# Performance work log

Hardware: AMD Instinct MI355X
Metric: run time of the kernel (lower is better)

## Reference

```python
import jax, jax.numpy as jnp
import numpy as np

N = 100000   # nodes
E = 1600000  # edges (avg degree 16)
D = 128      # feature dim (layer_sizes = [128, 128, 128])


def setup_inputs() -> dict:
    key = jax.random.key(0)
    ks = jax.random.split(key, 8)
    s = 1.0 / np.sqrt(D)  # glorot-ish scale for linear weights
    return {
        "x": jax.random.normal(ks[0], (N, D), jnp.float32),
        "edge_index": jax.random.randint(ks[1], (2, E), 0, N, dtype=jnp.int32),
        "perturb_first": jax.random.normal(ks[2], (N, D), jnp.float32) * 0.01,
        "perturb_last": jax.random.normal(ks[3], (N, D), jnp.float32) * 0.01,
        "W1": jax.random.normal(ks[4], (D, D), jnp.float32) * s,
        "b1": jnp.zeros((D,), jnp.float32),
        "W2": jax.random.normal(ks[5], (D, D), jnp.float32) * s,
        "b2": jnp.zeros((D,), jnp.float32),
    }


def reference(x, edge_index, perturb_first, perturb_last, W1, b1, W2, b2):
    n = x.shape[0]
    # PyG GCNConv: add self-loops, symmetric deg^{-1/2} normalization.
    loop = jnp.arange(n, dtype=edge_index.dtype)
    src = jnp.concatenate([edge_index[0], loop])  # [E+N]
    dst = jnp.concatenate([edge_index[1], loop])  # [E+N]
    deg = jax.ops.segment_sum(jnp.ones(dst.shape[0], x.dtype), dst, num_segments=n)
    dinv = jnp.where(deg > 0, 1.0 / jnp.sqrt(deg), 0.0)
    norm = (dinv[src] * dinv[dst])[:, None]  # [E+N, 1]

    def gcn_conv(h, W, b):
        h = h @ W.T                                   # linear (bias-free), [N, D]
        msg = h[src] * norm                           # gather + scale, [E+N, D]
        out = jax.ops.segment_sum(msg, dst, num_segments=n)  # scatter-add
        return out + b

    # forward only runs model[0] and model[3] (the two GCNConv layers);
    # norms and PReLU are skipped by the original forward.
    h = gcn_conv(x, W1, b1) + perturb_first
    out = gcn_conv(h, W2, b2) + perturb_last
    return out
```

## Files before the change

### kernel.cpp

```cpp
#include <hip/hip_runtime.h>
#include <math.h>

#define D 128
#define WS_PAD 132

typedef short bf16x8 __attribute__((ext_vector_type(8)));
typedef float f32x4 __attribute__((ext_vector_type(4)));

__device__ __forceinline__ unsigned short f2bf(float f) {
  unsigned u = __float_as_uint(f);
  u += 0x7FFFu + ((u >> 16) & 1u);
  return (unsigned short)(u >> 16);
}

__device__ __forceinline__ float bf2f(unsigned short h) {
  return __uint_as_float(((unsigned)h) << 16);
}

__device__ __forceinline__ float bflo(unsigned u) { return __uint_as_float(u << 16); }
__device__ __forceinline__ float bfhi(unsigned u) { return __uint_as_float(u & 0xFFFF0000u); }


__global__ __launch_bounds__(256) void wprep_kernel(const float* __restrict__ W2,
                                                    unsigned short* __restrict__ W2bf,
                                                    const float* __restrict__ W1,
                                                    unsigned short* __restrict__ W1h,
                                                    unsigned short* __restrict__ W1l) {
  int which = blockIdx.x;
  if (which < 8) {
    int t = which * 256 + threadIdx.x;
    #pragma unroll
    for (int q = 0; q < 2; ++q) {
      int idx = t + q * 2048;
      float4 w = ((const float4*)W2)[idx];
      ushort4 o;
      o.x = f2bf(w.x); o.y = f2bf(w.y); o.z = f2bf(w.z); o.w = f2bf(w.w);
      ((ushort4*)W2bf)[idx] = o;
    }
  } else {
    int t = (which - 8) * 256 + threadIdx.x;
    #pragma unroll
    for (int q = 0; q < 2; ++q) {
      int idx = t + q * 2048;
      float4 w = ((const float4*)W1)[idx];
      ushort4 hi, lo;
      hi.x = f2bf(w.x); lo.x = f2bf(w.x - bf2f(hi.x));
      hi.y = f2bf(w.y); lo.y = f2bf(w.y - bf2f(hi.y));
      hi.z = f2bf(w.z); lo.z = f2bf(w.z - bf2f(hi.z));
      hi.w = f2bf(w.w); lo.w = f2bf(w.w - bf2f(hi.w));
      ((ushort4*)W1h)[idx] = hi;
      ((ushort4*)W1l)[idx] = lo;
    }
  }
}


#define FUSED_GRID 2048
#define G1_PITCH 136

__global__ __launch_bounds__(256) void count_gemm1_kernel(
    const int* __restrict__ dst, int E, int* __restrict__ deg, int* __restrict__ rank,
    const float* __restrict__ X,
    const unsigned short* __restrict__ W1h, const unsigned short* __restrict__ W1l,
    unsigned short* __restrict__ H, int n) {
  __shared__ unsigned short Ths[32 * G1_PITCH];
  __shared__ unsigned short Tls[32 * G1_PITCH];
  int sub = blockIdx.x & 7;
  if (sub < 4) {
    int cb = (blockIdx.x >> 3) * 4 + sub;
    const int T4 = 1024 * 256 * 4;
    int t = cb * 256 + threadIdx.x;
    const bool al16 = ((E & 3) == 0);
    for (int e0 = t * 4; e0 < E; e0 += T4) {
      if (e0 + 4 <= E && al16) {
        int4 d = *(const int4*)(dst + e0);
        int r0 = atomicAdd(&deg[d.x], 1);
        int r1 = atomicAdd(&deg[d.y], 1);
        int r2 = atomicAdd(&deg[d.z], 1);
        int r3 = atomicAdd(&deg[d.w], 1);
        *(int4*)(rank + e0) = make_int4(r0, r1, r2, r3);
      } else {
        for (int e = e0; e < E && e < e0 + 4; ++e) rank[e] = atomicAdd(&deg[dst[e]], 1);
      }
    }
  } else {
    int gb = (blockIdx.x >> 3) * 4 + (sub - 4);
    const int tid = threadIdx.x;
    const int wv = tid >> 6;
    const int lane = tid & 63;
    const int m = lane & 15;
    const int quad = lane >> 4;
    const int mt = wv >> 1;
    const int ntb = (wv & 1) * 4;
    const int ntiles = (n + 31) >> 5;

    for (int tile = gb; tile < ntiles; tile += 1024) {
      const int row0 = tile << 5;
      const int rows_here = min(32, n - row0);
      __syncthreads();
      {
        const float4* Xg = (const float4*)(X + (size_t)row0 * D);
        int tmax = rows_here * 32;
        for (int t = tid; t < tmax; t += 256) {
          float4 xv = Xg[t];
          int r = t >> 5, c4 = (t & 31) << 2;
          ushort4 hi, lo;
          hi.x = f2bf(xv.x); lo.x = f2bf(xv.x - bf2f(hi.x));
          hi.y = f2bf(xv.y); lo.y = f2bf(xv.y - bf2f(hi.y));
          hi.z = f2bf(xv.z); lo.z = f2bf(xv.z - bf2f(hi.z));
          hi.w = f2bf(xv.w); lo.w = f2bf(xv.w - bf2f(hi.w));
          *(ushort4*)&Ths[r * G1_PITCH + c4] = hi;
          *(ushort4*)&Tls[r * G1_PITCH + c4] = lo;
        }
      }
      __syncthreads();

      f32x4 acc0 = {0.f, 0.f, 0.f, 0.f};
      f32x4 acc1 = {0.f, 0.f, 0.f, 0.f};
      f32x4 acc2 = {0.f, 0.f, 0.f, 0.f};
      f32x4 acc3 = {0.f, 0.f, 0.f, 0.f};
      #pragma unroll
      for (int s = 0; s < 4; ++s) {
        int k = (s << 5) + (quad << 3);
        bf16x8 ah = *(const bf16x8*)&Ths[(mt * 16 + m) * G1_PITCH + k];
        bf16x8 al = *(const bf16x8*)&Tls[(mt * 16 + m) * G1_PITCH + k];
        bf16x8 bh0 = *(const bf16x8*)&W1h[(size_t)((ntb + 0) * 16 + m) * 128 + k];
        bf16x8 bl0 = *(const bf16x8*)&W1l[(size_t)((ntb + 0) * 16 + m) * 128 + k];
        acc0 = __builtin_amdgcn_mfma_f32_16x16x32_bf16(ah, bh0, acc0, 0, 0, 0);
        acc0 = __builtin_amdgcn_mfma_f32_16x16x32_bf16(al, bh0, acc0, 0, 0, 0);
        acc0 = __builtin_amdgcn_mfma_f32_16x16x32_bf16(ah, bl0, acc0, 0, 0, 0);
        bf16x8 bh1 = *(const bf16x8*)&W1h[(size_t)((ntb + 1) * 16 + m) * 128 + k];
        bf16x8 bl1 = *(const bf16x8*)&W1l[(size_t)((ntb + 1) * 16 + m) * 128 + k];
        acc1 = __builtin_amdgcn_mfma_f32_16x16x32_bf16(ah, bh1, acc1, 0, 0, 0);
        acc1 = __builtin_amdgcn_mfma_f32_16x16x32_bf16(al, bh1, acc1, 0, 0, 0);
        acc1 = __builtin_amdgcn_mfma_f32_16x16x32_bf16(ah, bl1, acc1, 0, 0, 0);
        bf16x8 bh2 = *(const bf16x8*)&W1h[(size_t)((ntb + 2) * 16 + m) * 128 + k];
        bf16x8 bl2 = *(const bf16x8*)&W1l[(size_t)((ntb + 2) * 16 + m) * 128 + k];
        acc2 = __builtin_amdgcn_mfma_f32_16x16x32_bf16(ah, bh2, acc2, 0, 0, 0);
        acc2 = __builtin_amdgcn_mfma_f32_16x16x32_bf16(al, bh2, acc2, 0, 0, 0);
        acc2 = __builtin_amdgcn_mfma_f32_16x16x32_bf16(ah, bl2, acc2, 0, 0, 0);
        bf16x8 bh3 = *(const bf16x8*)&W1h[(size_t)((ntb + 3) * 16 + m) * 128 + k];
        bf16x8 bl3 = *(const bf16x8*)&W1l[(size_t)((ntb + 3) * 16 + m) * 128 + k];
        acc3 = __builtin_amdgcn_mfma_f32_16x16x32_bf16(ah, bh3, acc3, 0, 0, 0);
        acc3 = __builtin_amdgcn_mfma_f32_16x16x32_bf16(al, bh3, acc3, 0, 0, 0);
        acc3 = __builtin_amdgcn_mfma_f32_16x16x32_bf16(ah, bl3, acc3, 0, 0, 0);
      }
      #pragma unroll
      for (int r = 0; r < 4; ++r) {
        int row = mt * 16 + (quad << 2) + r;
        int g = row0 + row;
        if (g < n) {
          H[(size_t)g * D + (ntb + 0) * 16 + m] = f2bf(acc0[r]);
          H[(size_t)g * D + (ntb + 1) * 16 + m] = f2bf(acc1[r]);
          H[(size_t)g * D + (ntb + 2) * 16 + m] = f2bf(acc2[r]);
          H[(size_t)g * D + (ntb + 3) * 16 + m] = f2bf(acc3[r]);
        }
      }
    }
  }
}


__global__ __launch_bounds__(256) void fill_kernel(const int* __restrict__ src,
                                                   const int* __restrict__ dst,
                                                   const int* __restrict__ ptr,
                                                   const int* __restrict__ rank,
                                                   int* __restrict__ csr, int E) {
  const int T8 = FUSED_GRID * 256 * 8;
  int t = blockIdx.x * 256 + threadIdx.x;
  const bool al16 = ((E & 3) == 0);
  for (int e0 = t * 8; e0 < E; e0 += T8) {
    if (e0 + 8 <= E && al16) {
      int4 d0 = ((const int4*)(dst + e0))[0];
      int4 d1 = ((const int4*)(dst + e0))[1];
      int4 s0 = ((const int4*)(src + e0))[0];
      int4 s1 = ((const int4*)(src + e0))[1];
      int4 r0 = ((const int4*)(rank + e0))[0];
      int4 r1 = ((const int4*)(rank + e0))[1];
      csr[ptr[d0.x] + r0.x] = s0.x;
      csr[ptr[d0.y] + r0.y] = s0.y;
      csr[ptr[d0.z] + r0.z] = s0.z;
      csr[ptr[d0.w] + r0.w] = s0.w;
      csr[ptr[d1.x] + r1.x] = s1.x;
      csr[ptr[d1.y] + r1.y] = s1.y;
      csr[ptr[d1.z] + r1.z] = s1.z;
      csr[ptr[d1.w] + r1.w] = s1.w;
    } else {
      for (int e = e0; e < E && e < e0 + 8; ++e)
        csr[ptr[dst[e]] + rank[e]] = src[e];
    }
  }
}


__global__ __launch_bounds__(256) void scan_blocksum_kernel(const int* __restrict__ deg, int n,
                                                            int* __restrict__ blockSums) {
  __shared__ int sm[256];
  int t = threadIdx.x;
  int i = blockIdx.x * 256 + t;
  sm[t] = (i < n) ? deg[i] : 0;
  __syncthreads();
  for (int off = 128; off > 0; off >>= 1) {
    if (t < off) sm[t] += sm[t + off];
    __syncthreads();
  }
  if (t == 0) blockSums[blockIdx.x] = sm[0];
}

__global__ __launch_bounds__(512) void scan_top_kernel(int* __restrict__ blockSums, int nb) {
  __shared__ int sm[512];
  int t = threadIdx.x;
  int v = (t < nb) ? blockSums[t] : 0;
  sm[t] = v;
  __syncthreads();
  for (int off = 1; off < 512; off <<= 1) {
    int x = (t >= off) ? sm[t - off] : 0;
    __syncthreads();
    sm[t] += x;
    __syncthreads();
  }
  if (t < nb) blockSums[t] = sm[t] - v;
}

__global__ __launch_bounds__(256) void scan_write_kernel(const int* __restrict__ deg, int n,
                                                         const int* __restrict__ blockSums,
                                                         int* __restrict__ ptr,
                                                         float* __restrict__ dinv) {
  __shared__ int sm[256];
  int t = threadIdx.x;
  int i = blockIdx.x * 256 + t;
  int v = (i < n) ? deg[i] : 0;
  sm[t] = v;
  __syncthreads();
  for (int off = 1; off < 256; off <<= 1) {
    int x = (t >= off) ? sm[t - off] : 0;
    __syncthreads();
    sm[t] += x;
    __syncthreads();
  }
  if (i < n) {
    int ex = blockSums[blockIdx.x] + sm[t] - v;
    ptr[i] = ex;
    dinv[i] = 1.0f / sqrtf((float)(v + 1));
    if (i == n - 1) ptr[n] = ex + v;
  }
}


__device__ __forceinline__ void gemm_body(const float* __restrict__ X,
                                          const float* __restrict__ W,
                                          const float* __restrict__ dinv,
                                          unsigned short* __restrict__ H, int n,
                                          int bid, int nblocks,
                                          float* __restrict__ Ws, float* __restrict__ Xs) {
  const int tid = threadIdx.x;
  const int tx = tid & 31;
  const int ty = tid >> 5;
  const int ntiles = (n + 31) >> 5;

  for (int tile = bid; tile < ntiles; tile += nblocks) {
    const int row0 = tile << 5;
    const int rows_here = min(32, n - row0);
    __syncthreads();
    {
      const float4* Xg = (const float4*)(X + (size_t)row0 * D);
      int tmax = rows_here * 32;
      for (int t = tid; t < tmax; t += 256) ((float4*)Xs)[t] = Xg[t];
    }
    float acc[4][4] = {{0.f}};
    #pragma unroll
    for (int kt = 0; kt < 128; kt += 64) {
      __syncthreads();
      for (int t = tid; t < 2048; t += 256) {
        int j  = t >> 4;
        int k4 = (t & 15) << 2;
        float4 w = ((const float4*)W)[j * 32 + (kt >> 2) + (t & 15)];
        Ws[(k4 + 0) * WS_PAD + j] = w.x;
        Ws[(k4 + 1) * WS_PAD + j] = w.y;
        Ws[(k4 + 2) * WS_PAD + j] = w.z;
        Ws[(k4 + 3) * WS_PAD + j] = w.w;
      }
      __syncthreads();
      #pragma unroll 4
      for (int k = 0; k < 64; ++k) {
        float4 w = *(const float4*)&Ws[k * WS_PAD + (tx << 2)];
        #pragma unroll
        for (int r = 0; r < 4; ++r) {
          float xv = Xs[(ty + 8 * r) * 128 + (kt + k)];
          acc[r][0] += xv * w.x;
          acc[r][1] += xv * w.y;
          acc[r][2] += xv * w.z;
          acc[r][3] += xv * w.w;
        }
      }
    }
    #pragma unroll
    for (int r = 0; r < 4; ++r) {
      int row = row0 + ty + 8 * r;
      if (row < n) {
        float s = dinv[row];
        unsigned h0 = f2bf(s * acc[r][0]);
        unsigned h1 = f2bf(s * acc[r][1]);
        unsigned h2 = f2bf(s * acc[r][2]);
        unsigned h3 = f2bf(s * acc[r][3]);
        ((uint2*)(H + (size_t)row * D))[tx] = make_uint2(h0 | (h1 << 16), h2 | (h3 << 16));
      }
    }
  }
}


__global__ __launch_bounds__(256) void count_legacy_kernel(const int* __restrict__ dst, int E,
                                                           int* __restrict__ deg) {
  int e = blockIdx.x * 256 + threadIdx.x;
  if (e < E) atomicAdd(&deg[dst[e]], 1);
}

__global__ __launch_bounds__(256) void fused_fill_gemm_kernel(
    const int* __restrict__ src, const int* __restrict__ dst,
    int* __restrict__ ptr, int* __restrict__ csr, int E,
    const float* __restrict__ X, const float* __restrict__ W,
    const float* __restrict__ dinv, unsigned short* __restrict__ H, int n) {
  __shared__ float Ws[64 * WS_PAD];
  __shared__ float Xs[32 * 128];
  int sub = blockIdx.x & 7;
  if (sub < 2) {
    int fb = (blockIdx.x >> 3) * 2 + sub;
    int stride = 512 * 256;
    for (int e = fb * 256 + threadIdx.x; e < E; e += stride) {
      int d = dst[e];
      int pos = atomicAdd(&ptr[d], 1);
      csr[pos] = src[e];
    }
  } else {
    int gb = (blockIdx.x >> 3) * 6 + (sub - 2);
    gemm_body(X, W, dinv, H, n, gb, 1536, Ws, Xs);
  }
}

__global__ __launch_bounds__(256) void gemm128_kernel(const float* __restrict__ X,
                                                      const float* __restrict__ W,
                                                      const float* __restrict__ dinv,
                                                      unsigned short* __restrict__ H, int n) {
  __shared__ float Ws[64 * WS_PAD];
  __shared__ float Xs[32 * 128];
  gemm_body(X, W, dinv, H, n, blockIdx.x, gridDim.x, Ws, Xs);
}

__device__ __forceinline__ void gather_row_legacy(const int* __restrict__ csr, int start, int end,
                                                  const unsigned* __restrict__ Hu,
                                                  int i, int lane, float& ax, float& ay) {
  unsigned v = Hu[(size_t)i * 64 + lane];
  ax = __uint_as_float(v << 16);
  ay = __uint_as_float(v & 0xFFFF0000u);
  for (int e = start; e < end; ++e) {
    unsigned w = Hu[(size_t)csr[e] * 64 + lane];
    ax += __uint_as_float(w << 16);
    ay += __uint_as_float(w & 0xFFFF0000u);
  }
}

__global__ __launch_bounds__(256, 8) void gather_kernel_old(const int* __restrict__ csr,
                                                            const int* __restrict__ rend,
                                                            const float* __restrict__ dinv,
                                                            const unsigned* __restrict__ Hu,
                                                            const float* __restrict__ bias,
                                                            const float* __restrict__ perturb,
                                                            float* __restrict__ out, int n) {
  int i = (blockIdx.x << 2) + (threadIdx.x >> 6);
  if (i >= n) return;
  int lane = threadIdx.x & 63;
  int start = (i == 0) ? 0 : rend[i - 1];
  float ax, ay;
  gather_row_legacy(csr, start, rend[i], Hu, i, lane, ax, ay);
  float di = dinv[i];
  float2 p = ((const float2*)(perturb + (size_t)i * D))[lane];
  float2 o;
  o.x = bias[2 * lane + 0] + p.x + di * ax;
  o.y = bias[2 * lane + 1] + p.y + di * ay;
  ((float2*)(out + (size_t)i * D))[lane] = o;
}


__device__ __forceinline__ void gather_quad(const int* __restrict__ csr, int start, int end,
                                            const uint4* __restrict__ Hu4, int i, int sub,
                                            float acc[8]) {
  uint4 v = Hu4[(size_t)i * 16 + sub];
  acc[0] = bflo(v.x); acc[1] = bfhi(v.x);
  acc[2] = bflo(v.y); acc[3] = bfhi(v.y);
  acc[4] = bflo(v.z); acc[5] = bfhi(v.z);
  acc[6] = bflo(v.w); acc[7] = bfhi(v.w);
  int e = start;
  while (__ballot(e < end)) {
    uint4 w0 = {0u, 0u, 0u, 0u}, w1 = {0u, 0u, 0u, 0u};
    if (e < end)     w0 = Hu4[(size_t)csr[e] * 16 + sub];
    if (e + 1 < end) w1 = Hu4[(size_t)csr[e + 1] * 16 + sub];
    acc[0] += bflo(w0.x); acc[1] += bfhi(w0.x);
    acc[2] += bflo(w0.y); acc[3] += bfhi(w0.y);
    acc[4] += bflo(w0.z); acc[5] += bfhi(w0.z);
    acc[6] += bflo(w0.w); acc[7] += bfhi(w0.w);
    acc[0] += bflo(w1.x); acc[1] += bfhi(w1.x);
    acc[2] += bflo(w1.y); acc[3] += bfhi(w1.y);
    acc[4] += bflo(w1.z); acc[5] += bfhi(w1.z);
    acc[6] += bflo(w1.w); acc[7] += bfhi(w1.w);
    e += 2;
  }
}

__device__ __forceinline__ void gather_quad_w(const int* __restrict__ csr, int start, int end,
                                              const uint4* __restrict__ Hu4,
                                              const float* __restrict__ dinv,
                                              int i, int sub, float acc[8]) {
  float ds = dinv[i];
  uint4 v = Hu4[(size_t)i * 16 + sub];
  acc[0] = ds * bflo(v.x); acc[1] = ds * bfhi(v.x);
  acc[2] = ds * bflo(v.y); acc[3] = ds * bfhi(v.y);
  acc[4] = ds * bflo(v.z); acc[5] = ds * bfhi(v.z);
  acc[6] = ds * bflo(v.w); acc[7] = ds * bfhi(v.w);
  int e = start;
  while (__ballot(e < end)) {
    uint4 w0 = {0u, 0u, 0u, 0u}, w1 = {0u, 0u, 0u, 0u};
    float d0 = 0.f, d1 = 0.f;
    if (e < end)     { int j = csr[e];     w0 = Hu4[(size_t)j * 16 + sub]; d0 = dinv[j]; }
    if (e + 1 < end) { int j = csr[e + 1]; w1 = Hu4[(size_t)j * 16 + sub]; d1 = dinv[j]; }
    acc[0] += d0 * bflo(w0.x); acc[1] += d0 * bfhi(w0.x);
    acc[2] += d0 * bflo(w0.y); acc[3] += d0 * bfhi(w0.y);
    acc[4] += d0 * bflo(w0.z); acc[5] += d0 * bfhi(w0.z);
    acc[6] += d0 * bflo(w0.w); acc[7] += d0 * bfhi(w0.w);
    acc[0] += d1 * bflo(w1.x); acc[1] += d1 * bfhi(w1.x);
    acc[2] += d1 * bflo(w1.y); acc[3] += d1 * bfhi(w1.y);
    acc[4] += d1 * bflo(w1.z); acc[5] += d1 * bfhi(w1.z);
    acc[6] += d1 * bflo(w1.w); acc[7] += d1 * bfhi(w1.w);
    e += 2;
  }
}


__global__ __launch_bounds__(256, 8) void gather_kernel(const int* __restrict__ csr,
                                                        const int* __restrict__ rptr,
                                                        const float* __restrict__ dinv,
                                                        const unsigned* __restrict__ Hu,
                                                        const float* __restrict__ bias,
                                                        const float* __restrict__ perturb,
                                                        float* __restrict__ out, int n) {
  const int lane = threadIdx.x & 63;
  const int g = lane >> 4;
  const int sub = lane & 15;
  int i = (blockIdx.x << 4) + ((threadIdx.x >> 6) << 2) + g;
  bool valid = i < n;
  int ic = valid ? i : (n - 1);
  int start = rptr[ic];
  int end = valid ? rptr[ic + 1] : start;
  float acc[8];
  gather_quad(csr, start, end, (const uint4*)Hu, ic, sub, acc);
  if (valid) {
    float di = dinv[i];
    float4 b0 = *(const float4*)&bias[sub * 8];
    float4 b1 = *(const float4*)&bias[sub * 8 + 4];
    float4 p0 = *(const float4*)&perturb[(size_t)i * D + sub * 8];
    float4 p1 = *(const float4*)&perturb[(size_t)i * D + sub * 8 + 4];
    float4 o0, o1;
    o0.x = b0.x + p0.x + di * acc[0];
    o0.y = b0.y + p0.y + di * acc[1];
    o0.z = b0.z + p0.z + di * acc[2];
    o0.w = b0.w + p0.w + di * acc[3];
    o1.x = b1.x + p1.x + di * acc[4];
    o1.y = b1.y + p1.y + di * acc[5];
    o1.z = b1.z + p1.z + di * acc[6];
    o1.w = b1.w + p1.w + di * acc[7];
    *(float4*)&out[(size_t)i * D + sub * 8] = o0;
    *(float4*)&out[(size_t)i * D + sub * 8 + 4] = o1;
  }
}


#define GG_PITCH 136

__global__ __launch_bounds__(512, 8) void gather_gemm_kernel(
    const int* __restrict__ csr, const int* __restrict__ rptr,
    const float* __restrict__ dinv, const unsigned* __restrict__ Hu,
    const float* __restrict__ bias, const float* __restrict__ perturb,
    const unsigned short* __restrict__ W2bf, unsigned short* __restrict__ H2, int n) {
  __shared__ unsigned short Ts[32 * GG_PITCH];
  const int tid = threadIdx.x;
  const int wv = tid >> 6;
  const int lane = tid & 63;
  const int base = blockIdx.x << 5;

  {
    const int g = lane >> 4;
    const int sub = lane & 15;
    int row_in_block = (wv << 2) + g;
    int i = base + row_in_block;
    bool valid = i < n;
    int ic = valid ? i : (n - 1);
    int start = rptr[ic];
    int end = valid ? rptr[ic + 1] : start;
    float acc[8];
    gather_quad_w(csr, start, end, (const uint4*)Hu, dinv, ic, sub, acc);
    if (valid) {
      float di = dinv[i];
      float4 b0 = *(const float4*)&bias[sub * 8];
      float4 b1 = *(const float4*)&bias[sub * 8 + 4];
      float4 p0 = *(const float4*)&perturb[(size_t)i * D + sub * 8];
      float4 p1 = *(const float4*)&perturb[(size_t)i * D + sub * 8 + 4];
      unsigned q0 = (unsigned)f2bf(b0.x + p0.x + di * acc[0]) |
                    ((unsigned)f2bf(b0.y + p0.y + di * acc[1]) << 16);
      unsigned q1 = (unsigned)f2bf(b0.z + p0.z + di * acc[2]) |
                    ((unsigned)f2bf(b0.w + p0.w + di * acc[3]) << 16);
      unsigned q2 = (unsigned)f2bf(b1.x + p1.x + di * acc[4]) |
                    ((unsigned)f2bf(b1.y + p1.y + di * acc[5]) << 16);
      unsigned q3 = (unsigned)f2bf(b1.z + p1.z + di * acc[6]) |
                    ((unsigned)f2bf(b1.w + p1.w + di * acc[7]) << 16);
      uint4 pack = make_uint4(q0, q1, q2, q3);
      *(uint4*)&Ts[row_in_block * GG_PITCH + sub * 8] = pack;
    }
  }
  __syncthreads();

  const int mt = wv >> 2;
  const int nt0 = wv & 3;
  const int m = lane & 15;
  const int quad = lane >> 4;
  const unsigned short* Wrow0 = W2bf + (size_t)(nt0 * 16 + m) * 128;
  const unsigned short* Wrow1 = W2bf + (size_t)((nt0 + 4) * 16 + m) * 128;
  f32x4 acc0 = {0.f, 0.f, 0.f, 0.f};
  f32x4 acc1 = {0.f, 0.f, 0.f, 0.f};
  #pragma unroll
  for (int s = 0; s < 4; ++s) {
    int k = (s << 5) + (quad << 3);
    bf16x8 a  = *(const bf16x8*)&Ts[(mt * 16 + m) * GG_PITCH + k];
    bf16x8 b0 = *(const bf16x8*)&Wrow0[k];
    bf16x8 b1 = *(const bf16x8*)&Wrow1[k];
    acc0 = __builtin_amdgcn_mfma_f32_16x16x32_bf16(a, b0, acc0, 0, 0, 0);
    acc1 = __builtin_amdgcn_mfma_f32_16x16x32_bf16(a, b1, acc1, 0, 0, 0);
  }
  #pragma unroll
  for (int r = 0; r < 4; ++r) {
    int row = mt * 16 + (quad << 2) + r;
    int gg = base + row;
    if (gg < n) {
      float s = dinv[gg];
      H2[(size_t)gg * D + nt0 * 16 + m]       = f2bf(s * acc0[r]);
      H2[(size_t)gg * D + (nt0 + 4) * 16 + m] = f2bf(s * acc1[r]);
    }
  }
}


extern "C" void kernel_launch(void* const* d_in, const int* in_sizes, int n_in,
                              void* d_out, int out_size, void* d_ws, size_t ws_size,
                              hipStream_t stream) {
  const float* x  = (const float*)d_in[0];
  const int*   ei = (const int*)d_in[1];
  const float* pf = (const float*)d_in[2];
  const float* pl = (const float*)d_in[3];
  const float* W1 = (const float*)d_in[4];
  const float* b1 = (const float*)d_in[5];
  const float* W2 = (const float*)d_in[6];
  const float* b2 = (const float*)d_in[7];
  float* out = (float*)d_out;

  const int n = in_sizes[0] / D;
  const int E = in_sizes[1] / 2;
  const int* src = ei;
  const int* dst = ei + E;

  int*   deg       = (int*)d_ws;
  float* dinv      = (float*)d_ws + n;
  int*   ptr       = (int*)d_ws + 2 * n;
  int*   blockSums = (int*)d_ws + 3 * n + 1;
  int*   csr       = (int*)d_ws + 3 * n + 1 + 512;
  size_t a1_off = ((size_t)(3 * n + 1 + 512 + E) * 4 + 255) & ~(size_t)255;
  unsigned short* A1 = (unsigned short*)((char*)d_ws + a1_off);
  unsigned short* A2 = A1 + (size_t)n * D;
  unsigned short* W2bf = A2 + (size_t)n * D;
  unsigned short* W1h  = W2bf + 128 * 128;
  unsigned short* W1l  = W1h + 128 * 128;
  int* rank = (int*)A2;
  size_t needed = a1_off + (2 * (size_t)n * D + 3 * 128 * 128) * sizeof(unsigned short);
  const bool fused_l2 = (ws_size >= needed);

  const int nb_n = (n + 255) / 256;
  const int nb_e = (E + 255) / 256;
  const int nb_g16 = (n + 15) / 16;
  const int nb_g4 = (n + 3) / 4;

  hipMemsetAsync(deg, 0, (size_t)n * sizeof(int), stream);

  if (fused_l2) {
    wprep_kernel<<<16, 256, 0, stream>>>(W2, W2bf, W1, W1h, W1l);
    count_gemm1_kernel<<<FUSED_GRID, 256, 0, stream>>>(dst, E, deg, rank, x, W1h, W1l, A1, n);
    scan_blocksum_kernel<<<nb_n, 256, 0, stream>>>(deg, n, blockSums);
    scan_top_kernel<<<1, 512, 0, stream>>>(blockSums, nb_n);
    scan_write_kernel<<<nb_n, 256, 0, stream>>>(deg, n, blockSums, ptr, dinv);
    fill_kernel<<<FUSED_GRID, 256, 0, stream>>>(src, dst, ptr, rank, csr, E);
    gather_gemm_kernel<<<(n + 31) / 32, 512, 0, stream>>>(csr, ptr, dinv, (const unsigned*)A1,
                                                          b1, pf, W2bf, A2, n);
    gather_kernel<<<nb_g16, 256, 0, stream>>>(csr, ptr, dinv, (const unsigned*)A2, b2, pl, out, n);
  } else {
    count_legacy_kernel<<<nb_e, 256, 0, stream>>>(dst, E, deg);
    scan_blocksum_kernel<<<nb_n, 256, 0, stream>>>(deg, n, blockSums);
    scan_top_kernel<<<1, 512, 0, stream>>>(blockSums, nb_n);
    scan_write_kernel<<<nb_n, 256, 0, stream>>>(deg, n, blockSums, ptr, dinv);
    fused_fill_gemm_kernel<<<FUSED_GRID, 256, 0, stream>>>(src, dst, ptr, csr, E, x, W1, dinv, A1, n);
    gather_kernel_old<<<nb_g4, 256, 0, stream>>>(csr, ptr, dinv, (const unsigned*)A1, b1, pf, out, n);
    gemm128_kernel<<<1024, 256, 0, stream>>>(out, W2, dinv, A1, n);
    gather_kernel_old<<<nb_g4, 256, 0, stream>>>(csr, ptr, dinv, (const unsigned*)A1, b2, pl, out, n);
  }
}
```

Baseline: 460.2 us.

## Store layer-2 features in column slices and gather per slice for cache locality

The fused gather-GEMM kernel now writes H2 as eight column slices of 16 features each, and the final aggregation runs one block group per slice, with two lanes per node. Each slice's feature table is small enough to stay cache-resident during random neighbor gathers, which is meant to cut DRAM traffic for the irregular loads. In exchange, CSR indices and row pointers are read once per slice, and each gather fetches only 32 bytes per neighbor.

```diff
diff --git a/kernel.cpp b/kernel.cpp
--- a/kernel.cpp
+++ b/kernel.cpp
@@ -382,31 +382,6 @@
 }
 
 
-__device__ __forceinline__ void gather_quad(const int* __restrict__ csr, int start, int end,
-                                            const uint4* __restrict__ Hu4, int i, int sub,
-                                            float acc[8]) {
-  uint4 v = Hu4[(size_t)i * 16 + sub];
-  acc[0] = bflo(v.x); acc[1] = bfhi(v.x);
-  acc[2] = bflo(v.y); acc[3] = bfhi(v.y);
-  acc[4] = bflo(v.z); acc[5] = bfhi(v.z);
-  acc[6] = bflo(v.w); acc[7] = bfhi(v.w);
-  int e = start;
-  while (__ballot(e < end)) {
-    uint4 w0 = {0u, 0u, 0u, 0u}, w1 = {0u, 0u, 0u, 0u};
-    if (e < end)     w0 = Hu4[(size_t)csr[e] * 16 + sub];
-    if (e + 1 < end) w1 = Hu4[(size_t)csr[e + 1] * 16 + sub];
-    acc[0] += bflo(w0.x); acc[1] += bfhi(w0.x);
-    acc[2] += bflo(w0.y); acc[3] += bfhi(w0.y);
-    acc[4] += bflo(w0.z); acc[5] += bfhi(w0.z);
-    acc[6] += bflo(w0.w); acc[7] += bfhi(w0.w);
-    acc[0] += bflo(w1.x); acc[1] += bfhi(w1.x);
-    acc[2] += bflo(w1.y); acc[3] += bfhi(w1.y);
-    acc[4] += bflo(w1.z); acc[5] += bfhi(w1.z);
-    acc[6] += bflo(w1.w); acc[7] += bfhi(w1.w);
-    e += 2;
-  }
-}
-
 __device__ __forceinline__ void gather_quad_w(const int* __restrict__ csr, int start, int end,
                                               const uint4* __restrict__ Hu4,
                                               const float* __restrict__ dinv,
@@ -436,29 +411,53 @@
 }
 
 
-__global__ __launch_bounds__(256, 8) void gather_kernel(const int* __restrict__ csr,
-                                                        const int* __restrict__ rptr,
-                                                        const float* __restrict__ dinv,
-                                                        const unsigned* __restrict__ Hu,
-                                                        const float* __restrict__ bias,
-                                                        const float* __restrict__ perturb,
-                                                        float* __restrict__ out, int n) {
-  const int lane = threadIdx.x & 63;
-  const int g = lane >> 4;
-  const int sub = lane & 15;
-  int i = (blockIdx.x << 4) + ((threadIdx.x >> 6) << 2) + g;
+__global__ __launch_bounds__(256, 8) void gather2_sliced_kernel(
+    const int* __restrict__ csr, const int* __restrict__ rptr,
+    const float* __restrict__ dinv, const unsigned short* __restrict__ A2s,
+    const float* __restrict__ bias, const float* __restrict__ perturb,
+    float* __restrict__ out, int n) {
+  const int s = blockIdx.x & 7;
+  const int tile = blockIdx.x >> 3;
+  const int tid = threadIdx.x;
+  const int wv = tid >> 6;
+  const int lane = tid & 63;
+  const int pair = lane >> 1;
+  const int half = lane & 1;
+  int i = (tile << 7) + (wv << 5) + pair;
   bool valid = i < n;
   int ic = valid ? i : (n - 1);
   int start = rptr[ic];
   int end = valid ? rptr[ic + 1] : start;
+  const uint4* base = (const uint4*)(A2s + (size_t)s * n * 16);
+
+  uint4 v = base[(size_t)ic * 2 + half];
   float acc[8];
-  gather_quad(csr, start, end, (const uint4*)Hu, ic, sub, acc);
+  acc[0] = bflo(v.x); acc[1] = bfhi(v.x);
+  acc[2] = bflo(v.y); acc[3] = bfhi(v.y);
+  acc[4] = bflo(v.z); acc[5] = bfhi(v.z);
+  acc[6] = bflo(v.w); acc[7] = bfhi(v.w);
+  int e = start;
+  while (__ballot(e < end)) {
+    uint4 w0 = {0u, 0u, 0u, 0u}, w1 = {0u, 0u, 0u, 0u};
+    if (e < end)     w0 = base[(size_t)csr[e] * 2 + half];
+    if (e + 1 < end) w1 = base[(size_t)csr[e + 1] * 2 + half];
+    acc[0] += bflo(w0.x); acc[1] += bfhi(w0.x);
+    acc[2] += bflo(w0.y); acc[3] += bfhi(w0.y);
+    acc[4] += bflo(w0.z); acc[5] += bfhi(w0.z);
+    acc[6] += bflo(w0.w); acc[7] += bfhi(w0.w);
+    acc[0] += bflo(w1.x); acc[1] += bfhi(w1.x);
+    acc[2] += bflo(w1.y); acc[3] += bfhi(w1.y);
+    acc[4] += bflo(w1.z); acc[5] += bfhi(w1.z);
+    acc[6] += bflo(w1.w); acc[7] += bfhi(w1.w);
+    e += 2;
+  }
   if (valid) {
     float di = dinv[i];
-    float4 b0 = *(const float4*)&bias[sub * 8];
-    float4 b1 = *(const float4*)&bias[sub * 8 + 4];
-    float4 p0 = *(const float4*)&perturb[(size_t)i * D + sub * 8];
-    float4 p1 = *(const float4*)&perturb[(size_t)i * D + sub * 8 + 4];
+    int col = (s << 4) + (half << 3);
+    float4 b0 = *(const float4*)&bias[col];
+    float4 b1 = *(const float4*)&bias[col + 4];
+    float4 p0 = *(const float4*)&perturb[(size_t)i * D + col];
+    float4 p1 = *(const float4*)&perturb[(size_t)i * D + col + 4];
     float4 o0, o1;
     o0.x = b0.x + p0.x + di * acc[0];
     o0.y = b0.y + p0.y + di * acc[1];
@@ -468,8 +467,8 @@
     o1.y = b1.y + p1.y + di * acc[5];
     o1.z = b1.z + p1.z + di * acc[6];
     o1.w = b1.w + p1.w + di * acc[7];
-    *(float4*)&out[(size_t)i * D + sub * 8] = o0;
-    *(float4*)&out[(size_t)i * D + sub * 8 + 4] = o1;
+    *(float4*)&out[(size_t)i * D + col] = o0;
+    *(float4*)&out[(size_t)i * D + col + 4] = o1;
   }
 }
 
@@ -480,7 +479,7 @@
     const int* __restrict__ csr, const int* __restrict__ rptr,
     const float* __restrict__ dinv, const unsigned* __restrict__ Hu,
     const float* __restrict__ bias, const float* __restrict__ perturb,
-    const unsigned short* __restrict__ W2bf, unsigned short* __restrict__ H2, int n) {
+    const unsigned short* __restrict__ W2bf, unsigned short* __restrict__ H2s, int n) {
   __shared__ unsigned short Ts[32 * GG_PITCH];
   const int tid = threadIdx.x;
   const int wv = tid >> 6;
@@ -540,9 +539,9 @@
     int row = mt * 16 + (quad << 2) + r;
     int gg = base + row;
     if (gg < n) {
-      float s = dinv[gg];
-      H2[(size_t)gg * D + nt0 * 16 + m]       = f2bf(s * acc0[r]);
-      H2[(size_t)gg * D + (nt0 + 4) * 16 + m] = f2bf(s * acc1[r]);
+      float sc = dinv[gg];
+      H2s[(size_t)nt0 * n * 16 + (size_t)gg * 16 + m]       = f2bf(sc * acc0[r]);
+      H2s[(size_t)(nt0 + 4) * n * 16 + (size_t)gg * 16 + m] = f2bf(sc * acc1[r]);
     }
   }
 }
@@ -583,7 +582,6 @@
 
   const int nb_n = (n + 255) / 256;
   const int nb_e = (E + 255) / 256;
-  const int nb_g16 = (n + 15) / 16;
   const int nb_g4 = (n + 3) / 4;
 
   hipMemsetAsync(deg, 0, (size_t)n * sizeof(int), stream);
@@ -597,7 +595,8 @@
     fill_kernel<<<FUSED_GRID, 256, 0, stream>>>(src, dst, ptr, rank, csr, E);
     gather_gemm_kernel<<<(n + 31) / 32, 512, 0, stream>>>(csr, ptr, dinv, (const unsigned*)A1,
                                                           b1, pf, W2bf, A2, n);
-    gather_kernel<<<nb_g16, 256, 0, stream>>>(csr, ptr, dinv, (const unsigned*)A2, b2, pl, out, n);
+    int ntiles2 = (n + 127) / 128;
+    gather2_sliced_kernel<<<ntiles2 * 8, 256, 0, stream>>>(csr, ptr, dinv, A2, b2, pl, out, n);
   } else {
     count_legacy_kernel<<<nb_e, 256, 0, stream>>>(dst, E, deg);
     scan_blocksum_kernel<<<nb_n, 256, 0, stream>>>(deg, n, blockSums);
```

Result: slower. 524.0 us (+13.9%).
